# Kernel optimization log

Hardware: AMD Instinct MI355X
Metric: run time of the kernel (lower is better)

Reference implementation:

```python
import jax, jax.numpy as jnp
import numpy as np

DIM = 1024
N_HEADS = 16
HEAD_DIM = DIM // N_HEADS
COND_DIM = 1024
MLP_RATIO = 4
B, S = 4, 1024
LN_EPS = 1e-5


def _layer_norm(x, w):
    # F.layer_norm without affine bias, then * weight (per original LayerNorm)
    x32 = x.astype(jnp.float32)
    mu = jnp.mean(x32, axis=-1, keepdims=True)
    var = jnp.var(x32, axis=-1, keepdims=True)
    return (x32 - mu) * jax.lax.rsqrt(var + LN_EPS) * w


def _rope(t, cos, sin):
    # t: [b, s, h, d]; cos/sin: [s, d/2]; rotate-half convention
    d2 = t.shape[-1] // 2
    t1, t2 = t[..., :d2], t[..., d2:]
    c = cos[None, :, None, :]
    s = sin[None, :, None, :]
    return jnp.concatenate([t1 * c - t2 * s, t2 * c + t1 * s], axis=-1)


def setup_inputs() -> dict:
    key = jax.random.key(0)
    ks = jax.random.split(key, 12)
    inv_freq = 1.0 / (10000.0 ** (np.arange(0, HEAD_DIM, 2) / HEAD_DIM))
    ang = np.arange(S)[:, None] * inv_freq[None, :]
    return {
        "x": jax.random.normal(ks[0], (B, S, DIM), jnp.float32),
        "cos": jnp.asarray(np.cos(ang), jnp.float32),
        "sin": jnp.asarray(np.sin(ang), jnp.float32),
        "c": jax.random.normal(ks[1], (B, COND_DIM), jnp.float32),
        "w_ln1": jnp.ones((DIM,), jnp.float32),
        "w_ln2": jnp.ones((DIM,), jnp.float32),
        "w_qkv": jax.random.normal(ks[2], (DIM, 3 * DIM), jnp.float32) * 0.02,
        "w_attn_out": jax.random.normal(ks[3], (DIM, DIM), jnp.float32) * 0.02,
        "w_mlp1": jax.random.normal(ks[4], (DIM, MLP_RATIO * DIM), jnp.float32) * 0.02,
        "b_mlp1": jnp.zeros((MLP_RATIO * DIM,), jnp.float32),
        "w_mlp2": jax.random.normal(ks[5], (MLP_RATIO * DIM, DIM), jnp.float32) * 0.02,
        "b_mlp2": jnp.zeros((DIM,), jnp.float32),
        "w_ada": jax.random.normal(ks[6], (COND_DIM, 6 * DIM), jnp.float32) * 0.02,
        "b_ada": jax.random.normal(ks[7], (6 * DIM,), jnp.float32) * 0.02,
    }


def reference(x, cos, sin, c, w_ln1, w_ln2, w_qkv, w_attn_out,
              w_mlp1, b_mlp1, w_mlp2, b_mlp2, w_ada, b_ada):
    b, s, dim = x.shape
    # adaLN modulation: [b, 6*dim] -> six [b, 1, dim] chunks
    mod = (c @ w_ada + b_ada)[:, None, :]
    shift_msa, scale_msa, gate_msa, shift_mlp, scale_mlp, gate_mlp = jnp.split(mod, 6, axis=2)

    x_skip = x
    h = _layer_norm(x, w_ln1) * (1.0 + scale_msa) + shift_msa
    qkv = (h @ w_qkv).reshape(b, s, 3, N_HEADS, HEAD_DIM)
    q = _rope(qkv[:, :, 0], cos, sin)
    k = _rope(qkv[:, :, 1], cos, sin)
    v = qkv[:, :, 2]

    scale = 1.0 / jnp.sqrt(jnp.asarray(HEAD_DIM, x.dtype))
    scores = jnp.einsum('bshd,bthd->bhst', q, k) * scale  # [b,h,s,s]
    attn = jax.nn.softmax(scores, axis=-1)
    o = jnp.einsum('bhst,bthd->bshd', attn, v).reshape(b, s, dim)

    x = x_skip + gate_msa * (o @ w_attn_out)

    h2 = _layer_norm(x, w_ln2) * (1.0 + scale_mlp) + shift_mlp
    m = jax.nn.gelu(h2 @ w_mlp1 + b_mlp1, approximate=True) @ w_mlp2 + b_mlp2
    return x + gate_mlp * m
```

## Files before the change

kernel.cpp:

```cpp
#include <hip/hip_runtime.h>
#include <stdint.h>

typedef unsigned short u16;
typedef __bf16 bf16x8 __attribute__((ext_vector_type(8)));
typedef float f32x4 __attribute__((ext_vector_type(4)));

#define MOD6  6144

__device__ __forceinline__ float b2f(unsigned int u) {
    union { unsigned int i; float f; } z; z.i = u << 16; return z.f;
}
__device__ __forceinline__ u16 f2b(float f) {
    union { float f; unsigned int i; } z; z.f = f;
    unsigned int i = z.i;
    return (u16)((i + 0x7fffu + ((i >> 16) & 1u)) >> 16);
}
union U4 { uint4 u; u16 s[8]; };
union U2 { uint2 u; u16 s[4]; };
union B8 { bf16x8 v; unsigned int w[4]; };

__device__ __forceinline__ float ldf(const void* p, size_t i, int isbf) {
    if (isbf) return b2f(((const u16*)p)[i]);
    return ((const float*)p)[i];
}
__device__ __forceinline__ void load4(const void* p, size_t i, int isbf, float* v) {
    if (isbf) {
        U2 t; t.u = *(const uint2*)((const u16*)p + i);
#pragma unroll
        for (int e = 0; e < 4; e++) v[e] = b2f(t.s[e]);
    } else {
        float4 f = *(const float4*)((const float*)p + i);
        v[0] = f.x; v[1] = f.y; v[2] = f.z; v[3] = f.w;
    }
}

__device__ __forceinline__ void gld16(u16* lds, const u16* g) {
    __builtin_amdgcn_global_load_lds(
        (__attribute__((address_space(1))) void*)(g),
        (__attribute__((address_space(3))) void*)(lds), 16, 0, 0);
}

__global__ void detect_dtype(const unsigned int* __restrict__ w, int* __restrict__ flag) {
    if (threadIdx.x == 0 && blockIdx.x == 0)
        *flag = (w[0] == 0x3F803F80u) ? 1 : 0;
}

__global__ void transpose_any(const void* __restrict__ in, u16* __restrict__ out,
                              int K, int N, const int* __restrict__ flag) {
    const int isbf = *flag;
    __shared__ u16 tile[64][66];
    const int ntn = N >> 6;
    const int k0 = (blockIdx.x / ntn) << 6;
    const int n0 = (blockIdx.x % ntn) << 6;
    const int tid = threadIdx.x;
    const int r = tid >> 3;
    const int c = (tid & 7) * 8;
#pragma unroll
    for (int rr = 0; rr < 64; rr += 32) {
        const size_t base = (size_t)(k0 + r + rr) * N + n0 + c;
        u16* t = &tile[r + rr][c];
        if (isbf) {
            U4 v; v.u = *(const uint4*)((const u16*)in + base);
#pragma unroll
            for (int e = 0; e < 8; e++) t[e] = v.s[e];
        } else {
            float4 a = *(const float4*)((const float*)in + base);
            float4 b = *(const float4*)((const float*)in + base + 4);
            t[0] = f2b(a.x); t[1] = f2b(a.y); t[2] = f2b(a.z); t[3] = f2b(a.w);
            t[4] = f2b(b.x); t[5] = f2b(b.y); t[6] = f2b(b.z); t[7] = f2b(b.w);
        }
    }
    __syncthreads();
#pragma unroll
    for (int rr = 0; rr < 64; rr += 32) {
        U4 v;
#pragma unroll
        for (int e = 0; e < 8; e++) v.s[e] = tile[c + e][r + rr];
        *(uint4*)&out[(size_t)(n0 + r + rr) * K + k0 + c] = v.u;
    }
}

__global__ void ada_partial(const void* __restrict__ c, const void* __restrict__ w_ada,
                            float* __restrict__ part, const int* __restrict__ flag) {
    const int isbf = *flag;
    const int g = blockIdx.x * 256 + threadIdx.x;
    const int slice = g / 24576;
    const int idx = g - slice * 24576;
    const int b = idx / MOD6, n = idx - (idx / MOD6) * MOD6;
    const int k0 = slice * 128;
    float acc = 0.f;
    if (isbf) {
        const u16* cr = (const u16*)c + b * 1024 + k0;
        const u16* wp = (const u16*)w_ada + (size_t)k0 * MOD6 + n;
#pragma unroll 8
        for (int k = 0; k < 128; k++)
            acc += b2f(cr[k]) * b2f(wp[(size_t)k * MOD6]);
    } else {
        const float* cr = (const float*)c + b * 1024 + k0;
        const float* wp = (const float*)w_ada + (size_t)k0 * MOD6 + n;
#pragma unroll 8
        for (int k = 0; k < 128; k++)
            acc += cr[k] * wp[(size_t)k * MOD6];
    }
    part[g] = acc;
}
__global__ void ada_reduce(const float* __restrict__ part, const void* __restrict__ b_ada,
                           float* __restrict__ mod, const int* __restrict__ flag) {
    const int g = blockIdx.x * 256 + threadIdx.x;
    float acc = ldf(b_ada, g % MOD6, *flag);
#pragma unroll
    for (int s = 0; s < 8; s++) acc += part[s * 24576 + g];
    mod[g] = acc;
}

__global__ void ln_mod_kernel(const void* __restrict__ x, const void* __restrict__ w,
                              const float* __restrict__ mod, int shift_off,
                              int scale_off, u16* __restrict__ out,
                              const int* __restrict__ flag, int x_is_f32) {
    const int isbf = *flag;
    const int xb = x_is_f32 ? 0 : isbf;
    const int tk = blockIdx.x;
    const int b = tk >> 10;
    const int tid = threadIdx.x;
    float v[4];
    load4(x, (size_t)tk * 1024 + tid * 4, xb, v);
    float s = v[0] + v[1] + v[2] + v[3];
    float ss = v[0]*v[0] + v[1]*v[1] + v[2]*v[2] + v[3]*v[3];
#pragma unroll
    for (int off = 1; off < 64; off <<= 1) {
        s  += __shfl_xor(s, off);
        ss += __shfl_xor(ss, off);
    }
    __shared__ float ls[4], lss[4];
    if ((tid & 63) == 0) { ls[tid >> 6] = s; lss[tid >> 6] = ss; }
    __syncthreads();
    s  = ls[0] + ls[1] + ls[2] + ls[3];
    ss = lss[0] + lss[1] + lss[2] + lss[3];
    const float mu  = s * (1.f / 1024.f);
    const float var = ss * (1.f / 1024.f) - mu * mu;
    const float rstd = rsqrtf(var + 1e-5f);
    float wv[4];
    load4(w, (size_t)tid * 4, isbf, wv);
    const float* mb = mod + (size_t)b * MOD6;
    U2 o;
#pragma unroll
    for (int e = 0; e < 4; e++) {
        const int col = tid * 4 + e;
        float n = (v[e] - mu) * rstd * wv[e];
        o.s[e] = f2b(n * (1.f + mb[scale_off + col]) + mb[shift_off + col]);
    }
    *(uint2*)(out + (size_t)tk * 1024 + tid * 4) = o.u;
}

__global__ void out_init(const float* __restrict__ res, const float* __restrict__ gate,
                         const void* __restrict__ bias, float* __restrict__ out,
                         const int* __restrict__ flag) {
    const int isbf = *flag;
    const int g = blockIdx.x * 256 + threadIdx.x;
    const int col = (g & 255) * 4;
    const int row = g >> 8;
    const int b = row >> 10;
    float bv[4];
    load4(bias, (size_t)col, isbf, bv);
    const float* gp = gate + (size_t)b * MOD6 + col;
    float4 r = *(const float4*)(res + (size_t)row * 1024 + col);
    float4 o;
    o.x = r.x + gp[0] * bv[0];
    o.y = r.y + gp[1] * bv[1];
    o.z = r.z + gp[2] * bv[2];
    o.w = r.w + gp[3] * bv[3];
    *(float4*)(out + (size_t)row * 1024 + col) = o;
}

__global__ void copy_f32(const void* __restrict__ x, float* __restrict__ out,
                         const int* __restrict__ flag) {
    const int isbf = *flag;
    const int g = blockIdx.x * 256 + threadIdx.x;
    float v[4];
    load4(x, (size_t)g * 4, isbf, v);
    float4 o; o.x = v[0]; o.y = v[1]; o.z = v[2]; o.w = v[3];
    *(float4*)(out + (size_t)g * 4) = o;
}

#define EPI_STORE 0
#define EPI_GELU_BIAS 2
#define EPI_ATOMIC_GATE 4

template <int EPI>
__launch_bounds__(512, 2)
__global__ void gemm_bt(const u16* __restrict__ A, const u16* __restrict__ Bt,
                        void* __restrict__ Cv, int M, int N, int K,
                        const void* __restrict__ res, const float* __restrict__ gate,
                        const void* __restrict__ bias, const int* __restrict__ flag,
                        int Ks) {
    __shared__ __align__(16) u16 sA[2][256 * 32];
    __shared__ __align__(16) u16 sB[2][256 * 32];
    const int isbf = flag ? *flag : 0;
    const int tid = threadIdx.x;
    const int lane = tid & 63;
    const int w = tid >> 6;
    const int wm = w >> 2, wn = w & 3;
    const int c16 = lane & 15, quad = lane >> 4;

    int bx, by, bz;
    {
        const int nx = gridDim.x, ny = gridDim.y, nz = gridDim.z;
        const int flat = blockIdx.x + nx * (blockIdx.y + ny * blockIdx.z);
        const int q = flat & 7;
        const int s = flat >> 3;
        const int g = s / nx;
        bx = s - g * nx;
        const int p = q * ((ny * nz) >> 3) + g;
        by = p % ny;
        bz = p / ny;
    }
    const int m0 = by * 256, n0 = bx * 256;
    const int kt0 = bz * Ks;

    const int srow = tid >> 2;
    const int schunk = tid & 3;
    const int gchunk = schunk ^ (srow & 3);

    const u16* gA = A + (size_t)m0 * K + 8 * gchunk + kt0;
    const u16* gB = Bt + (size_t)n0 * K + 8 * gchunk + kt0;
    const int cs = quad ^ (c16 & 3);

    const int r0 = srow;
    const int r1 = srow + 128;
    const int d0 = r0 * 32 + 8 * schunk;
    const int d1 = r1 * 32 + 8 * schunk;

    f32x4 acc[8][4];
#pragma unroll
    for (int i = 0; i < 8; i++)
#pragma unroll
        for (int j = 0; j < 4; j++) acc[i][j] = (f32x4){0.f, 0.f, 0.f, 0.f};

    gld16(&sA[0][d0], gA + (size_t)r0 * K);
    gld16(&sA[0][d1], gA + (size_t)r1 * K);
    gld16(&sB[0][d0], gB + (size_t)r0 * K);
    gld16(&sB[0][d1], gB + (size_t)r1 * K);
    __syncthreads();

    const int nt = Ks >> 5;
    int cur = 0;
#pragma unroll 1
    for (int t = 0; t < nt; ++t) {
        if (t + 1 < nt) {
            const int kt = (t + 1) << 5;
            u16* dA = &sA[cur ^ 1][0];
            u16* dB = &sB[cur ^ 1][0];
            gld16(dA + d0, gA + (size_t)r0 * K + kt);
            gld16(dA + d1, gA + (size_t)r1 * K + kt);
            gld16(dB + d0, gB + (size_t)r0 * K + kt);
            gld16(dB + d1, gB + (size_t)r1 * K + kt);
        }
        const u16* fA = &sA[cur][0];
        const u16* fB = &sB[cur][0];
        bf16x8 af[8], bfr[4];
#pragma unroll
        for (int i = 0; i < 8; i++)
            af[i] = *(const bf16x8*)&fA[(128 * wm + 16 * i + c16) * 32 + 8 * cs];
#pragma unroll
        for (int j = 0; j < 4; j++)
            bfr[j] = *(const bf16x8*)&fB[(64 * wn + 16 * j + c16) * 32 + 8 * cs];
#pragma unroll
        for (int i = 0; i < 8; i++)
#pragma unroll
            for (int j = 0; j < 4; j++)
                acc[i][j] = __builtin_amdgcn_mfma_f32_16x16x32_bf16(
                    af[i], bfr[j], acc[i][j], 0, 0, 0);
        __syncthreads();
        cur ^= 1;
    }

#pragma unroll
    for (int i = 0; i < 8; i++) {
#pragma unroll
        for (int r = 0; r < 4; r++) {
            const int row = m0 + 128 * wm + 16 * i + 4 * quad + r;
            const int b = row >> 10;
#pragma unroll
            for (int j = 0; j < 4; j++) {
                const int col = n0 + 64 * wn + 16 * j + c16;
                float v = acc[i][j][r];
                if constexpr (EPI == EPI_GELU_BIAS) {
                    v += ldf(bias, col, isbf);
                    const float u = 0.7978845608f * (v + 0.044715f * v * v * v);
                    const float e = __expf(2.f * u);
                    const float t = 1.f - 2.f / (e + 1.f);
                    v = 0.5f * v * (1.f + t);
                }
                if constexpr (EPI == EPI_ATOMIC_GATE) {
                    atomicAdd((float*)Cv + (size_t)row * N + col,
                              gate[(size_t)b * MOD6 + col] * v);
                } else {
                    ((u16*)Cv)[(size_t)row * N + col] = f2b(v);
                }
            }
        }
    }
}

__global__ void rope_kernel(u16* __restrict__ qkv, const void* __restrict__ cosb,
                            const void* __restrict__ sinb, const int* __restrict__ flag) {
    const int isbf = *flag;
    const int g = blockIdx.x * 256 + threadIdx.x;
    const int q8 = g & 7;
    const int h = (g >> 3) & 15;
    const int tk = g >> 7;
    const int s = tk & 1023;
    const int d = q8 * 4;
    u16* row = qkv + (size_t)tk * 3072;

    float c4[4], s4[4];
    load4(cosb, (size_t)s * 32 + d, isbf, c4);
    load4(sinb, (size_t)s * 32 + d, isbf, s4);

#pragma unroll
    for (int which = 0; which < 2; which++) {
        u16* p1 = row + which * 1024 + h * 64 + d;
        u16* p2 = p1 + 32;
        U2 t1, t2;
        t1.u = *(const uint2*)p1;
        t2.u = *(const uint2*)p2;
        U2 o1, o2;
#pragma unroll
        for (int e = 0; e < 4; e++) {
            const float a = b2f(t1.s[e]), bb = b2f(t2.s[e]);
            o1.s[e] = f2b(a * c4[e] - bb * s4[e]);
            o2.s[e] = f2b(bb * c4[e] + a * s4[e]);
        }
        *(uint2*)p1 = o1.u;
        *(uint2*)p2 = o2.u;
    }
}

__launch_bounds__(256, 4)
__global__ void attn_mfma(const u16* __restrict__ qkv, u16* __restrict__ o_out) {
    __shared__ __align__(16) u16 sK[64 * 72];
    __shared__ __align__(16) u16 sVt[64 * 72];
    const int flat = blockIdx.x;
    const int xq = flat & 7, xs = flat >> 3;
    const int qt = xs & 15;
    const int bh = xq * 8 + (xs >> 4);
    const int b = bh >> 4, h = bh & 15;
    const int tid = threadIdx.x;
    const int w = tid >> 6;
    const int lane = tid & 63;
    const int c = lane & 15;
    const int quad = lane >> 4;

    const int q0 = qt * 64 + w * 16;
    bf16x8 qf0, qf1;
    {
        const u16* qrow = qkv + (size_t)(b * 1024 + q0 + c) * 3072 + h * 64;
        qf0 = *(const bf16x8*)(qrow + quad * 8);
        qf1 = *(const bf16x8*)(qrow + 32 + quad * 8);
    }
    f32x4 of[4];
#pragma unroll
    for (int dt = 0; dt < 4; dt++) of[dt] = (f32x4){0.f, 0.f, 0.f, 0.f};
    float mI = -1e30f, lI = 0.f;

    const int skey = tid >> 3;
    const int sch  = tid & 7;
    const int src0 = (((2 * quad) & 3) << 4) + c;
    const int src1 = (((2 * quad + 1) & 3) << 4) + c;

#pragma unroll 1
    for (int kt = 0; kt < 1024; kt += 64) {
        __syncthreads();
#pragma unroll
        for (int p = 0; p < 2; p++) {
            const int key = skey + p * 32;
            const u16* krow = qkv + (size_t)(b * 1024 + kt + key) * 3072 + 1024
                              + h * 64 + sch * 8;
            uint4 kv = *(const uint4*)krow;
            *(uint4*)&sK[key * 72 + sch * 8] = kv;
            U4 vv; vv.u = *(const uint4*)(krow + 1024);
#pragma unroll
            for (int e = 0; e < 8; e++) sVt[(sch * 8 + e) * 72 + key] = vv.s[e];
        }
        __syncthreads();
#pragma unroll
        for (int ks = 0; ks < 64; ks += 32) {
            bf16x8 k00 = *(const bf16x8*)&sK[(ks + c) * 72 + quad * 8];
            bf16x8 k01 = *(const bf16x8*)&sK[(ks + c) * 72 + 32 + quad * 8];
            bf16x8 k10 = *(const bf16x8*)&sK[(ks + 16 + c) * 72 + quad * 8];
            bf16x8 k11 = *(const bf16x8*)&sK[(ks + 16 + c) * 72 + 32 + quad * 8];
            f32x4 s0 = (f32x4){0.f, 0.f, 0.f, 0.f};
            f32x4 s1 = (f32x4){0.f, 0.f, 0.f, 0.f};
            s0 = __builtin_amdgcn_mfma_f32_16x16x32_bf16(k00, qf0, s0, 0, 0, 0);
            s0 = __builtin_amdgcn_mfma_f32_16x16x32_bf16(k01, qf1, s0, 0, 0, 0);
            s1 = __builtin_amdgcn_mfma_f32_16x16x32_bf16(k10, qf0, s1, 0, 0, 0);
            s1 = __builtin_amdgcn_mfma_f32_16x16x32_bf16(k11, qf1, s1, 0, 0, 0);
            float sc[8];
#pragma unroll
            for (int r = 0; r < 4; r++) { sc[r] = s0[r] * 0.125f; sc[4 + r] = s1[r] * 0.125f; }
            float tm = sc[0];
#pragma unroll
            for (int j = 1; j < 8; j++) tm = fmaxf(tm, sc[j]);
            tm = fmaxf(tm, __shfl_xor(tm, 16));
            tm = fmaxf(tm, __shfl_xor(tm, 32));
            const float mNew = fmaxf(mI, tm);
            const float alpha = __expf(mI - mNew);
            float p8[8];
            float psum = 0.f;
#pragma unroll
            for (int j = 0; j < 8; j++) { p8[j] = __expf(sc[j] - mNew); psum += p8[j]; }
            psum += __shfl_xor(psum, 16);
            psum += __shfl_xor(psum, 32);
            lI = lI * alpha + psum;
            mI = mNew;
#pragma unroll
            for (int dt = 0; dt < 4; dt++) {
#pragma unroll
                for (int r = 0; r < 4; r++) of[dt][r] *= alpha;
            }
            const unsigned int a0 = (unsigned)f2b(p8[0]) | ((unsigned)f2b(p8[1]) << 16);
            const unsigned int a1 = (unsigned)f2b(p8[2]) | ((unsigned)f2b(p8[3]) << 16);
            const unsigned int b0 = (unsigned)f2b(p8[4]) | ((unsigned)f2b(p8[5]) << 16);
            const unsigned int b1 = (unsigned)f2b(p8[6]) | ((unsigned)f2b(p8[7]) << 16);
            const unsigned int xa0 = (unsigned)__shfl((int)a0, src0);
            const unsigned int xb0 = (unsigned)__shfl((int)b0, src0);
            const unsigned int xa1 = (unsigned)__shfl((int)a1, src0);
            const unsigned int xb1 = (unsigned)__shfl((int)b1, src0);
            const unsigned int ya0 = (unsigned)__shfl((int)a0, src1);
            const unsigned int yb0 = (unsigned)__shfl((int)b0, src1);
            const unsigned int ya1 = (unsigned)__shfl((int)a1, src1);
            const unsigned int yb1 = (unsigned)__shfl((int)b1, src1);
            B8 pf;
            pf.w[0] = quad < 2 ? xa0 : xb0;
            pf.w[1] = quad < 2 ? xa1 : xb1;
            pf.w[2] = quad < 2 ? ya0 : yb0;
            pf.w[3] = quad < 2 ? ya1 : yb1;
#pragma unroll
            for (int dt = 0; dt < 4; dt++) {
                bf16x8 vf = *(const bf16x8*)&sVt[(dt * 16 + c) * 72 + ks + quad * 8];
                of[dt] = __builtin_amdgcn_mfma_f32_16x16x32_bf16(vf, pf.v, of[dt], 0, 0, 0);
            }
        }
    }
    const float inv = 1.f / lI;
    const size_t orow = (size_t)(b * 1024 + q0 + c) * 1024 + h * 64;
#pragma unroll
    for (int dt = 0; dt < 4; dt++) {
        U2 pk;
#pragma unroll
        for (int r = 0; r < 4; r++) pk.s[r] = f2b(of[dt][r] * inv);
        *(uint2*)(o_out + orow + dt * 16 + quad * 4) = pk.u;
    }
}

extern "C" void kernel_launch(void* const* d_in, const int* in_sizes, int n_in,
                              void* d_out, int out_size, void* d_ws, size_t ws_size,
                              hipStream_t stream) {
    (void)in_sizes; (void)n_in; (void)out_size; (void)ws_size;
    const void* x      = d_in[0];
    const void* cosb   = d_in[1];
    const void* sinb   = d_in[2];
    const void* c      = d_in[3];
    const void* w_ln1  = d_in[4];
    const void* w_ln2  = d_in[5];
    const void* w_qkv  = d_in[6];
    const void* w_attn = d_in[7];
    const void* w_mlp1 = d_in[8];
    const void* b_mlp1 = d_in[9];
    const void* w_mlp2 = d_in[10];
    const void* b_mlp2 = d_in[11];
    const void* w_ada  = d_in[12];
    const void* b_ada  = d_in[13];
    char* ws = (char*)d_ws;

    u16*   wT_qkv  = (u16*)(ws + 0);
    u16*   wT_attn = (u16*)(ws + 6291456);
    u16*   wT_mlp1 = (u16*)(ws + 8388608);
    u16*   wT_mlp2 = (u16*)(ws + 16777216);
    float* mod     = (float*)(ws + 25165824);
    u16*   hbuf    = (u16*)(ws + 25264128);
    u16*   big     = (u16*)(ws + 33652736);
    float* x2      = (float*)(ws + 67207168);
    int*   flag    = (int*)(ws + 83984384);
    float* part    = (float*)big;

    detect_dtype<<<1, 64, 0, stream>>>((const unsigned int*)w_ln1, flag);
    transpose_any<<<dim3(16 * 48), 256, 0, stream>>>(w_qkv, wT_qkv, 1024, 3072, flag);
    transpose_any<<<dim3(16 * 16), 256, 0, stream>>>(w_attn, wT_attn, 1024, 1024, flag);
    transpose_any<<<dim3(16 * 64), 256, 0, stream>>>(w_mlp1, wT_mlp1, 1024, 4096, flag);
    transpose_any<<<dim3(64 * 16), 256, 0, stream>>>(w_mlp2, wT_mlp2, 4096, 1024, flag);
    ada_partial<<<768, 256, 0, stream>>>(c, w_ada, part, flag);
    ada_reduce<<<96, 256, 0, stream>>>(part, b_ada, mod, flag);
    ln_mod_kernel<<<4096, 256, 0, stream>>>(x, w_ln1, mod, 0, 1024, hbuf, flag, 0);
    gemm_bt<EPI_STORE><<<dim3(12, 16), 512, 0, stream>>>(
        hbuf, wT_qkv, big, 4096, 3072, 1024, nullptr, nullptr, nullptr, flag, 1024);
    rope_kernel<<<2048, 256, 0, stream>>>(big, cosb, sinb, flag);
    attn_mfma<<<1024, 256, 0, stream>>>(big, hbuf);
    copy_f32<<<4096, 256, 0, stream>>>(x, x2, flag);
    gemm_bt<EPI_ATOMIC_GATE><<<dim3(4, 16, 4), 512, 0, stream>>>(
        hbuf, wT_attn, x2, 4096, 1024, 1024, nullptr, mod + 2048, nullptr, flag, 256);
    ln_mod_kernel<<<4096, 256, 0, stream>>>(x2, w_ln2, mod, 3072, 4096, hbuf, flag, 1);
    out_init<<<4096, 256, 0, stream>>>(x2, mod + 5120, b_mlp2, (float*)d_out, flag);
    gemm_bt<EPI_GELU_BIAS><<<dim3(16, 16), 512, 0, stream>>>(
        hbuf, wT_mlp1, big, 4096, 4096, 1024, nullptr, nullptr, b_mlp1, flag, 1024);
    gemm_bt<EPI_ATOMIC_GATE><<<dim3(4, 16, 4), 512, 0, stream>>>(
        big, wT_mlp2, (float*)d_out, 4096, 1024, 4096, nullptr, mod + 5120, nullptr,
        flag, 1024);
}
```

Before: 535.1 us.

## Deepen GEMM shared-memory pipeline to four stages with explicit vmcnt waits

Replaces the double-buffered LDS pipeline in the bf16 MFMA GEMM with a four-buffer ring that prefetches three k-tiles ahead. It uses hand-placed s_waitcnt vmcnt and s_barrier instead of __syncthreads, and raises wave priority around the MFMA block. The goal is to hide global-load latency behind more compute. LDS use doubles to 128 KB per block, which may cut occupancy below the two blocks per CU the launch bounds request. The vmcnt counts also depend on how the compiler orders loads, so a wrong count could make the kernel read stale tiles.

```diff
diff --git a/kernel.cpp b/kernel.cpp
--- a/kernel.cpp
+++ b/kernel.cpp
@@ -193,8 +193,8 @@
                         const void* __restrict__ res, const float* __restrict__ gate,
                         const void* __restrict__ bias, const int* __restrict__ flag,
                         int Ks) {
-    __shared__ __align__(16) u16 sA[2][256 * 32];
-    __shared__ __align__(16) u16 sB[2][256 * 32];
+    __shared__ __align__(16) u16 sA[4][256 * 32];
+    __shared__ __align__(16) u16 sB[4][256 * 32];
     const int isbf = flag ? *flag : 0;
     const int tid = threadIdx.x;
     const int lane = tid & 63;
@@ -217,61 +217,71 @@
     const int m0 = by * 256, n0 = bx * 256;
     const int kt0 = bz * Ks;
 
-    const int srow = tid >> 2;
-    const int schunk = tid & 3;
-    const int gchunk = schunk ^ (srow & 3);
-
-    const u16* gA = A + (size_t)m0 * K + 8 * gchunk + kt0;
-    const u16* gB = Bt + (size_t)n0 * K + 8 * gchunk + kt0;
+    const int f0 = tid, f1 = tid + 512;
+    const int goff0 = (f0 >> 2) * K + 8 * ((f0 & 3) ^ ((f0 >> 2) & 3));
+    const int goff1 = (f1 >> 2) * K + 8 * ((f1 & 3) ^ ((f1 >> 2) & 3));
+    const int ldso0 = f0 * 8;
+    const int ldso1 = f1 * 8;
+
+    const u16* gA = A + (size_t)m0 * K + kt0;
+    const u16* gB = Bt + (size_t)n0 * K + kt0;
     const int cs = quad ^ (c16 & 3);
 
-    const int r0 = srow;
-    const int r1 = srow + 128;
-    const int d0 = r0 * 32 + 8 * schunk;
-    const int d1 = r1 * 32 + 8 * schunk;
-
     f32x4 acc[8][4];
 #pragma unroll
     for (int i = 0; i < 8; i++)
 #pragma unroll
         for (int j = 0; j < 4; j++) acc[i][j] = (f32x4){0.f, 0.f, 0.f, 0.f};
 
-    gld16(&sA[0][d0], gA + (size_t)r0 * K);
-    gld16(&sA[0][d1], gA + (size_t)r1 * K);
-    gld16(&sB[0][d0], gB + (size_t)r0 * K);
-    gld16(&sB[0][d1], gB + (size_t)r1 * K);
-    __syncthreads();
-
     const int nt = Ks >> 5;
-    int cur = 0;
+
+    asm volatile("s_waitcnt vmcnt(0)" ::: "memory");
+
+#pragma unroll
+    for (int pt = 0; pt < 3; ++pt) {
+        const int kt = pt << 5;
+        gld16(&sA[pt][ldso0], gA + goff0 + kt);
+        gld16(&sA[pt][ldso1], gA + goff1 + kt);
+        gld16(&sB[pt][ldso0], gB + goff0 + kt);
+        gld16(&sB[pt][ldso1], gB + goff1 + kt);
+    }
+    asm volatile("s_waitcnt vmcnt(8)\n\ts_barrier" ::: "memory");
+
 #pragma unroll 1
     for (int t = 0; t < nt; ++t) {
-        if (t + 1 < nt) {
-            const int kt = (t + 1) << 5;
-            u16* dA = &sA[cur ^ 1][0];
-            u16* dB = &sB[cur ^ 1][0];
-            gld16(dA + d0, gA + (size_t)r0 * K + kt);
-            gld16(dA + d1, gA + (size_t)r1 * K + kt);
-            gld16(dB + d0, gB + (size_t)r0 * K + kt);
-            gld16(dB + d1, gB + (size_t)r1 * K + kt);
-        }
-        const u16* fA = &sA[cur][0];
-        const u16* fB = &sB[cur][0];
+        if (t + 3 < nt) {
+            const int bi = (t + 3) & 3;
+            const int kt = (t + 3) << 5;
+            gld16(&sA[bi][ldso0], gA + goff0 + kt);
+            gld16(&sA[bi][ldso1], gA + goff1 + kt);
+            gld16(&sB[bi][ldso0], gB + goff0 + kt);
+            gld16(&sB[bi][ldso1], gB + goff1 + kt);
+        }
+        const u16* fA = &sA[t & 3][0];
+        const u16* fB = &sB[t & 3][0];
         bf16x8 af[8], bfr[4];
+#pragma unroll
+        for (int j = 0; j < 4; j++)
+            bfr[j] = *(const bf16x8*)&fB[(64 * wn + 16 * j + c16) * 32 + 8 * cs];
 #pragma unroll
         for (int i = 0; i < 8; i++)
             af[i] = *(const bf16x8*)&fA[(128 * wm + 16 * i + c16) * 32 + 8 * cs];
-#pragma unroll
-        for (int j = 0; j < 4; j++)
-            bfr[j] = *(const bf16x8*)&fB[(64 * wn + 16 * j + c16) * 32 + 8 * cs];
+        __builtin_amdgcn_s_setprio(1);
 #pragma unroll
         for (int i = 0; i < 8; i++)
 #pragma unroll
             for (int j = 0; j < 4; j++)
                 acc[i][j] = __builtin_amdgcn_mfma_f32_16x16x32_bf16(
                     af[i], bfr[j], acc[i][j], 0, 0, 0);
-        __syncthreads();
-        cur ^= 1;
+        __builtin_amdgcn_s_setprio(0);
+        const int rem = nt - 2 - t;
+        if (rem >= 2) {
+            asm volatile("s_waitcnt vmcnt(8)\n\ts_barrier" ::: "memory");
+        } else if (rem == 1) {
+            asm volatile("s_waitcnt vmcnt(4)\n\ts_barrier" ::: "memory");
+        } else if (rem == 0) {
+            asm volatile("s_waitcnt vmcnt(0)\n\ts_barrier" ::: "memory");
+        }
     }
 
 #pragma unroll
```

Result: no change. 532.8 us (-0.4%).
